# Performance work log

Measured on AMD Instinct MI355X. Metric: run time of the kernel, lower is better.

The kernel has to match this reference:

```python
import jax, jax.numpy as jnp
import numpy as np

NUM_FREQ = 4
MAX_FREQ_LOG2 = 10.0
# standard NeRF frequency bands: 2^linspace(0, max_freq_log2, num_freq)
FREQ_BANDS = 2.0 ** np.linspace(0.0, MAX_FREQ_LOG2, NUM_FREQ).astype(np.float32)


def positional_encoding(x):
    # x: [N, 3] -> [N, 3*(1 + 2*num_freq)] = [N, 27]
    xf = x[..., None, :] * jnp.asarray(FREQ_BANDS, dtype=x.dtype)[:, None]  # [N, F, 3]
    enc = jnp.concatenate([jnp.sin(xf), jnp.cos(xf)], axis=-1)  # [N, F, 6]
    return jnp.concatenate([x, enc.reshape(x.shape[0], -1)], axis=-1)


def setup_inputs() -> dict:
    key = jax.random.key(0)
    k1, k2, k3 = jax.random.split(key, 3)
    N = 2097152
    x = jax.random.normal(k1, (N, 3), dtype=jnp.float32)
    in_dim, hidden = 27, 32
    # torch Linear default init scale ~ 1/sqrt(fan_in)
    W1 = jax.random.normal(k2, (in_dim, hidden), dtype=jnp.float32) / np.sqrt(in_dim)
    b1 = jnp.zeros((hidden,), dtype=jnp.float32)
    W2 = jax.random.normal(k3, (hidden, 1), dtype=jnp.float32) / np.sqrt(hidden)
    b2 = jnp.zeros((1,), dtype=jnp.float32)
    return {"x": x, "W1": W1, "b1": b1, "W2": W2, "b2": b2}


def reference(x, W1, b1, W2, b2):
    t = positional_encoding(x)                    # [N, 27]
    h = jax.nn.relu(t @ W1 + b1)                  # [N, 32]
    out = jax.nn.relu(h @ W2 + b2)                # [N, 1]
    return out
```

## Files before the change

kernel.cpp:

```cpp
#include <hip/hip_runtime.h>


#define NPTS  2097152
#define BLOCK 256
#define TILES 4
#define NBLK  (NPTS / (BLOCK * TILES))

typedef __bf16 bf16x8 __attribute__((ext_vector_type(8)));
typedef float  f32x8  __attribute__((ext_vector_type(8)));
typedef float  f32x4  __attribute__((ext_vector_type(4)));

__global__ __launch_bounds__(BLOCK, 4) void nerf_mfma9(
    const float* __restrict__ x,
    const float* __restrict__ W1,
    const float* __restrict__ b1,
    const float* __restrict__ W2,
    const float* __restrict__ b2,
    float* __restrict__ out)
{
    const int tid  = threadIdx.x;
    const int wave = tid >> 6;
    const int lane = tid & 63;
    const int g    = lane >> 4;
    const int c    = lane & 15;

    const float INV2PI = 0.15915494309189535f;
    float Fg = 1.0f;
    Fg = (g == 1) ? 10.079368f : Fg;
    Fg = (g == 2) ? 101.59367f : Fg;
    Fg = (g == 3) ? 1024.0f    : Fg;
    Fg *= INV2PI;

    bf16x8 afrag[2];
    #pragma unroll
    for (int mt = 0; mt < 2; ++mt) {
        const int j = mt * 16 + c;
        f32x8 af;
        #pragma unroll
        for (int i = 0; i < 3; ++i)     af[i] = W1[(3 + 6 * g + i) * 32 + j];
        #pragma unroll
        for (int i = 3; i < 6; ++i)     af[i] = W1[(6 + 6 * g + (i - 3)) * 32 + j];
        af[6] = (g < 3) ? W1[g * 32 + j] : b1[j];
        af[7] = 0.0f;
        afrag[mt] = __builtin_convertvector(af, bf16x8);
    }

    bf16x8 a2;
    {
        f32x8 a2f;
        #pragma unroll
        for (int i = 0; i < 4; ++i) {
            a2f[i]     = W2[4 * g + i];
            a2f[4 + i] = W2[16 + 4 * g + i];
        }
        a2 = __builtin_convertvector(a2f, bf16x8);
    }
    const float bias2 = b2[0];

    const int tbase = blockIdx.x * (4 * TILES) + wave * TILES;

    #pragma unroll
    for (int t = 0; t < TILES; ++t) {
        const float3* xb3 = (const float3*)(x + (size_t)(tbase + t) * 192);
        float3 P[4];
        #pragma unroll
        for (int nt = 0; nt < 4; ++nt) P[nt] = xb3[16 * nt + c];

        float p[4];
        #pragma unroll
        for (int nt = 0; nt < 4; ++nt) {
            const float x0 = P[nt].x, x1 = P[nt].y, x2 = P[nt].z;

            const float a0  = __builtin_amdgcn_fractf(x0 * Fg);
            const float a1  = __builtin_amdgcn_fractf(x1 * Fg);
            const float a2r = __builtin_amdgcn_fractf(x2 * Fg);
            float extra = x0;
            extra = (g == 1) ? x1 : extra;
            extra = (g == 2) ? x2 : extra;
            extra = (g == 3) ? 1.0f : extra;

            f32x8 bff;
            bff[0] = __builtin_amdgcn_sinf(a0);
            bff[1] = __builtin_amdgcn_sinf(a1);
            bff[2] = __builtin_amdgcn_sinf(a2r);
            bff[3] = __builtin_amdgcn_cosf(a0);
            bff[4] = __builtin_amdgcn_cosf(a1);
            bff[5] = __builtin_amdgcn_cosf(a2r);
            bff[6] = extra;
            bff[7] = 0.0f;
            const bf16x8 bf = __builtin_convertvector(bff, bf16x8);

            f32x4 acc0 = {0.f, 0.f, 0.f, 0.f};
            f32x4 acc1 = {0.f, 0.f, 0.f, 0.f};
            acc0 = __builtin_amdgcn_mfma_f32_16x16x32_bf16(afrag[0], bf, acc0, 0, 0, 0);
            acc1 = __builtin_amdgcn_mfma_f32_16x16x32_bf16(afrag[1], bf, acc1, 0, 0, 0);

            f32x8 hf;
            #pragma unroll
            for (int r = 0; r < 4; ++r) {
                hf[r]     = fmaxf(acc0[r], 0.0f);
                hf[4 + r] = fmaxf(acc1[r], 0.0f);
            }
            const bf16x8 h8 = __builtin_convertvector(hf, bf16x8);
            f32x4 o = {0.f, 0.f, 0.f, 0.f};
            o = __builtin_amdgcn_mfma_f32_16x16x32_bf16(a2, h8, o, 0, 0, 0);
            p[nt] = o[0];
        }

        float v = p[0];
        v = (g == 1) ? p[1] : v;
        v = (g == 2) ? p[2] : v;
        v = (g == 3) ? p[3] : v;
        out[(size_t)(tbase + t) * 64 + lane] = fmaxf(v + bias2, 0.0f);
    }
}

extern "C" void kernel_launch(void* const* d_in, const int* in_sizes, int n_in,
                              void* d_out, int out_size, void* d_ws, size_t ws_size,
                              hipStream_t stream) {
    const float* x  = (const float*)d_in[0];
    const float* W1 = (const float*)d_in[1];
    const float* b1 = (const float*)d_in[2];
    const float* W2 = (const float*)d_in[3];
    const float* b2 = (const float*)d_in[4];
    float* out = (float*)d_out;

    nerf_mfma9<<<NBLK, BLOCK, 0, stream>>>(x, W1, b1, W2, b2, out);
}
```

Measured before the change: 19.86 us.

## Replace hardware sin/cos with shared-memory sine lookup table

Each block builds a 4096-entry sine table in LDS and replaces the fract plus sin/cos transcendental instructions with truncated-index table lookups, getting cosine from a quarter-period offset. Launch bounds are raised to 8 blocks per CU to allow more occupancy. The aim is to cut transcendental ALU cost. In exchange, every block rebuilds the table and hits a barrier, random LDS lookups can cause bank conflicts, and truncation lowers accuracy; results are then rounded to bf16 anyway.

Result: slower. 21.53 us (+8.4%).

```diff
diff --git a/kernel.cpp b/kernel.cpp
--- a/kernel.cpp
+++ b/kernel.cpp
@@ -5,12 +5,13 @@
 #define BLOCK 256
 #define TILES 4
 #define NBLK  (NPTS / (BLOCK * TILES))
+#define TABN  4096
 
 typedef __bf16 bf16x8 __attribute__((ext_vector_type(8)));
 typedef float  f32x8  __attribute__((ext_vector_type(8)));
 typedef float  f32x4  __attribute__((ext_vector_type(4)));
 
-__global__ __launch_bounds__(BLOCK, 4) void nerf_mfma9(
+__global__ __launch_bounds__(BLOCK, 8) void nerf_tab(
     const float* __restrict__ x,
     const float* __restrict__ W1,
     const float* __restrict__ b1,
@@ -18,18 +19,26 @@
     const float* __restrict__ b2,
     float* __restrict__ out)
 {
+    __shared__ float stab[TABN];
+
     const int tid  = threadIdx.x;
     const int wave = tid >> 6;
     const int lane = tid & 63;
     const int g    = lane >> 4;
     const int c    = lane & 15;
 
+    #pragma unroll
+    for (int i = 0; i < TABN / BLOCK; ++i) {
+        const int idx = tid + i * BLOCK;
+        stab[idx] = __builtin_amdgcn_sinf((float)idx * (1.0f / TABN));
+    }
+
     const float INV2PI = 0.15915494309189535f;
     float Fg = 1.0f;
     Fg = (g == 1) ? 10.079368f : Fg;
     Fg = (g == 2) ? 101.59367f : Fg;
     Fg = (g == 3) ? 1024.0f    : Fg;
-    Fg *= INV2PI;
+    const float FgN = Fg * INV2PI * (float)TABN;
 
     bf16x8 afrag[2];
     #pragma unroll
@@ -37,14 +46,13 @@
         const int j = mt * 16 + c;
         f32x8 af;
         #pragma unroll
-        for (int i = 0; i < 3; ++i)     af[i] = W1[(3 + 6 * g + i) * 32 + j];
+        for (int i = 0; i < 3; ++i) af[i] = W1[(3 + 6 * g + i) * 32 + j];
         #pragma unroll
-        for (int i = 3; i < 6; ++i)     af[i] = W1[(6 + 6 * g + (i - 3)) * 32 + j];
+        for (int i = 3; i < 6; ++i) af[i] = W1[(6 + 6 * g + (i - 3)) * 32 + j];
         af[6] = (g < 3) ? W1[g * 32 + j] : b1[j];
         af[7] = 0.0f;
         afrag[mt] = __builtin_convertvector(af, bf16x8);
     }
-
     bf16x8 a2;
     {
         f32x8 a2f;
@@ -56,6 +64,9 @@
         a2 = __builtin_convertvector(a2f, bf16x8);
     }
     const float bias2 = b2[0];
+    const f32x4 Z = {0.f, 0.f, 0.f, 0.f};
+
+    __syncthreads();
 
     const int tbase = blockIdx.x * (4 * TILES) + wave * TILES;
 
@@ -71,29 +82,30 @@
         for (int nt = 0; nt < 4; ++nt) {
             const float x0 = P[nt].x, x1 = P[nt].y, x2 = P[nt].z;
 
-            const float a0  = __builtin_amdgcn_fractf(x0 * Fg);
-            const float a1  = __builtin_amdgcn_fractf(x1 * Fg);
-            const float a2r = __builtin_amdgcn_fractf(x2 * Fg);
+            const int i0 = (int)(x0 * FgN);
+            const int i1 = (int)(x1 * FgN);
+            const int i2 = (int)(x2 * FgN);
+
             float extra = x0;
             extra = (g == 1) ? x1 : extra;
             extra = (g == 2) ? x2 : extra;
             extra = (g == 3) ? 1.0f : extra;
 
             f32x8 bff;
-            bff[0] = __builtin_amdgcn_sinf(a0);
-            bff[1] = __builtin_amdgcn_sinf(a1);
-            bff[2] = __builtin_amdgcn_sinf(a2r);
-            bff[3] = __builtin_amdgcn_cosf(a0);
-            bff[4] = __builtin_amdgcn_cosf(a1);
-            bff[5] = __builtin_amdgcn_cosf(a2r);
+            bff[0] = stab[i0 & (TABN - 1)];
+            bff[1] = stab[i1 & (TABN - 1)];
+            bff[2] = stab[i2 & (TABN - 1)];
+            bff[3] = stab[(i0 + TABN / 4) & (TABN - 1)];
+            bff[4] = stab[(i1 + TABN / 4) & (TABN - 1)];
+            bff[5] = stab[(i2 + TABN / 4) & (TABN - 1)];
             bff[6] = extra;
             bff[7] = 0.0f;
             const bf16x8 bf = __builtin_convertvector(bff, bf16x8);
 
-            f32x4 acc0 = {0.f, 0.f, 0.f, 0.f};
-            f32x4 acc1 = {0.f, 0.f, 0.f, 0.f};
-            acc0 = __builtin_amdgcn_mfma_f32_16x16x32_bf16(afrag[0], bf, acc0, 0, 0, 0);
-            acc1 = __builtin_amdgcn_mfma_f32_16x16x32_bf16(afrag[1], bf, acc1, 0, 0, 0);
+            const f32x4 acc0 =
+                __builtin_amdgcn_mfma_f32_16x16x32_bf16(afrag[0], bf, Z, 0, 0, 0);
+            const f32x4 acc1 =
+                __builtin_amdgcn_mfma_f32_16x16x32_bf16(afrag[1], bf, Z, 0, 0, 0);
 
             f32x8 hf;
             #pragma unroll
@@ -102,8 +114,8 @@
                 hf[4 + r] = fmaxf(acc1[r], 0.0f);
             }
             const bf16x8 h8 = __builtin_convertvector(hf, bf16x8);
-            f32x4 o = {0.f, 0.f, 0.f, 0.f};
-            o = __builtin_amdgcn_mfma_f32_16x16x32_bf16(a2, h8, o, 0, 0, 0);
+            const f32x4 o =
+                __builtin_amdgcn_mfma_f32_16x16x32_bf16(a2, h8, Z, 0, 0, 0);
             p[nt] = o[0];
         }
 
@@ -125,5 +137,5 @@
     const float* b2 = (const float*)d_in[4];
     float* out = (float*)d_out;
 
-    nerf_mfma9<<<NBLK, BLOCK, 0, stream>>>(x, W1, b1, W2, b2, out);
+    nerf_tab<<<NBLK, BLOCK, 0, stream>>>(x, W1, b1, W2, b2, out);
 }
```
